# Optimization experiments

Measured on AMD Instinct MI355X. Metric: run time of the kernel, lower is better.

## Reference

```python
import jax, jax.numpy as jnp
import numpy as np

T, B, S = 8, 4, 2048
LAT, SYM, NC = 1024, 256, 512


def setup_inputs() -> dict:
    key = jax.random.key(0)
    ks = jax.random.split(key, 16)
    inp = {
        "token_state": jax.random.normal(ks[0], (B, S, LAT), jnp.float32),
        "bus_symbols": jax.random.normal(ks[1], (T, B, S, SYM), jnp.float32),
        "bus_indices": jax.random.randint(ks[2], (T, B, S), 0, NC),
        "bus_outputs": jax.random.normal(ks[3], (T, B, S, LAT), jnp.float32),
        "bus_mask": jnp.zeros((T,), jnp.bool_),
        # parameters (stored as (in, out) matrices)
        "Wq": jax.random.normal(ks[4], (SYM, 1), jnp.float32) / np.sqrt(SYM),
        "bq": jnp.zeros((1,), jnp.float32),
        "Wread": jax.random.normal(ks[5], (2 * LAT, LAT), jnp.float32) / np.sqrt(2 * LAT),
        "bread": jnp.zeros((LAT,), jnp.float32),
        "Wsym": jax.random.normal(ks[6], (LAT, SYM), jnp.float32) / np.sqrt(LAT),
        "bsym": jnp.zeros((SYM,), jnp.float32),
        "Wc1": jax.random.normal(ks[7], (LAT + SYM, LAT), jnp.float32) / np.sqrt(LAT + SYM),
        "bc1": jnp.zeros((LAT,), jnp.float32),
        "Wc2": jax.random.normal(ks[8], (LAT, LAT), jnp.float32) / np.sqrt(LAT),
        "bc2": jnp.zeros((LAT,), jnp.float32),
        "codebook": jax.random.normal(ks[9], (NC, SYM), jnp.float32),
    }
    return inp


def reference(token_state, bus_symbols, bus_indices, bus_outputs, bus_mask,
              Wq, bq, Wread, bread, Wsym, bsym, Wc1, bc1, Wc2, bc2, codebook):
    Tm, Bb, Ss, Dsym = bus_symbols.shape
    N = Bb * Ss
    syms = bus_symbols.reshape(Tm, N, Dsym)          # [T, N, SYM]
    outs = bus_outputs.reshape(Tm, N, -1)            # [T, N, LAT]

    # top-1 bus message routing
    relevance = (syms @ Wq + bq)[..., 0]             # [T, N]
    top_msg_idx = jnp.argmax(relevance, axis=0)      # [N]
    chosen = jnp.take_along_axis(outs, top_msg_idx[None, :, None], axis=0)[0]  # [N, LAT]
    bus_context = chosen.reshape(Bb, Ss, -1)

    z = jnp.concatenate([token_state, bus_context], axis=-1)
    z_read = z @ Wread + bread                       # [B, S, LAT]
    raw_symbol = z_read @ Wsym + bsym                # [B, S, SYM]

    # VQ: cdist argmin (squared distance has same argmin)
    flat = raw_symbol.reshape(-1, Dsym)              # [N, SYM]
    d2 = (jnp.sum(flat * flat, axis=1, keepdims=True)
          - 2.0 * flat @ codebook.T
          + jnp.sum(codebook * codebook, axis=1)[None, :])  # [N, NC]
    indices = jnp.argmin(d2, axis=-1)                # [N]
    quantized = codebook[indices].reshape(Bb, Ss, Dsym)

    h = jax.nn.relu(jnp.concatenate([z_read, quantized], axis=-1) @ Wc1 + bc1)
    node_output = h @ Wc2 + bc2 + token_state

    used_counts = jnp.zeros((Tm,), jnp.int32).at[top_msg_idx].add(1)
    keep_mask = used_counts == 0
    return node_output, quantized, indices.reshape(Bb, Ss), keep_mask
```

## Files before the change

kernel.cpp:

```cpp
#include <hip/hip_runtime.h>
#include <hip/hip_bf16.h>

#define DEVI __device__ __forceinline__

namespace {

constexpr int T_   = 8;
constexpr int NTOK = 8192;
constexpr int LAT  = 1024;
constexpr int SYM  = 256;
constexpr int NC   = 512;
constexpr float TAU = 0.6f;

typedef short short8 __attribute__((ext_vector_type(8)));
typedef float floatx4 __attribute__((ext_vector_type(4)));

DEVI unsigned short f2bf(float f){
  union { float f; unsigned u; } v; v.f = f;
  return (unsigned short)((v.u + 0x7fffu + ((v.u >> 16) & 1u)) >> 16);
}

DEVI void gload_lds16(const void* g, void* l){
  __builtin_amdgcn_global_load_lds((const __attribute__((address_space(1))) void*)g,
                                   (__attribute__((address_space(3))) void*)l, 16, 0, 0);
}

__global__ void route_k(const float* __restrict__ syms, const float* __restrict__ Wq,
                        int* __restrict__ top, int* __restrict__ counts){
  int gt = blockIdx.x * blockDim.x + threadIdx.x;
  int wid = gt >> 6, lane = gt & 63;
  if (wid >= NTOK) return;
  float4 wq = *(const float4*)(Wq + lane * 4);
  float best = -INFINITY; int bt = 0;
  for (int t = 0; t < T_; ++t){
    float4 s = *(const float4*)(syms + ((size_t)t * NTOK + wid) * SYM + lane * 4);
    float p = s.x*wq.x + s.y*wq.y + s.z*wq.z + s.w*wq.w;
    #pragma unroll
    for (int off = 32; off; off >>= 1) p += __shfl_down(p, off, 64);
    p = __shfl(p, 0, 64);
    if (p > best){ best = p; bt = t; }
  }
  if (lane == 0){ top[wid] = bt; atomicAdd(&counts[bt], 1); }
}

__global__ void mask_k(const int* __restrict__ counts, float* __restrict__ out_mask){
  int t = threadIdx.x;
  if (t < T_) out_mask[t] = (counts[t] == 0) ? 1.0f : 0.0f;
}

__global__ void cbt_k(const float* __restrict__ cb, float* __restrict__ cbT){
  int i = blockIdx.x * blockDim.x + threadIdx.x;
  if (i < NC * SYM){ int c = i / SYM, k = i % SYM; cbT[k * NC + c] = cb[i]; }
}

__global__ void cnorm_k(const float* __restrict__ cb, const float* __restrict__ bsym,
                        float* __restrict__ cnorm, float* __restrict__ svec){
  int gt = blockIdx.x * blockDim.x + threadIdx.x;
  int wid = gt >> 6, lane = gt & 63;
  if (wid >= NC) return;
  float4 v = *(const float4*)(cb + (size_t)wid * SYM + lane * 4);
  float4 b = *(const float4*)(bsym + lane * 4);
  float p = v.x*v.x + v.y*v.y + v.z*v.z + v.w*v.w;
  float q = v.x*(v.x-2.f*b.x) + v.y*(v.y-2.f*b.y) + v.z*(v.z-2.f*b.z) + v.w*(v.w-2.f*b.w);
  #pragma unroll
  for (int off = 32; off; off >>= 1){ p += __shfl_down(p, off, 64); q += __shfl_down(q, off, 64); }
  if (lane == 0){ cnorm[wid] = p; svec[wid] = q; }
}

__global__ void rbias_k(const float* __restrict__ bread, const float* __restrict__ Wsym,
                        const float* __restrict__ bsym, float* __restrict__ rb){
  int t = threadIdx.x;
  float acc = bsym[t];
  for (int k = 0; k < LAT; ++k) acc += bread[k] * Wsym[(size_t)k * SYM + t];
  rb[t] = acc;
}

__global__ void t32_k(const float* __restrict__ in, unsigned short* __restrict__ out,
                      int R, int C){
  __shared__ float tile[32][33];
  int tid = threadIdx.x;
  int tx = tid & 31, ty = tid >> 5;
  int r0 = blockIdx.y * 32, c0 = blockIdx.x * 32;
  #pragma unroll
  for (int j = 0; j < 4; ++j)
    tile[ty + j*8][tx] = in[(size_t)(r0 + ty + j*8) * C + c0 + tx];
  __syncthreads();
  #pragma unroll
  for (int j = 0; j < 4; ++j)
    out[(size_t)(c0 + ty + j*8) * R + r0 + tx] = f2bf(tile[tx][ty + j*8]);
}

__global__ void pack_az(const float* __restrict__ ts, const float* __restrict__ bus,
                        const int* __restrict__ top, unsigned short* __restrict__ Az){
  int id = blockIdx.x * blockDim.x + threadIdx.x;
  int m = id >> 9, c = (id & 511) * 4;
  const float* src = (c < LAT) ? (ts + (size_t)m * LAT + c)
                               : (bus + ((size_t)top[m] * NTOK + m) * LAT + (c - LAT));
  float4 v = *(const float4*)src;
  ushort4 o; o.x = f2bf(v.x); o.y = f2bf(v.y); o.z = f2bf(v.z); o.w = f2bf(v.w);
  *(ushort4*)(Az + (size_t)m * (2*LAT) + c) = o;
}

template<int BM, int BN, int BK, int TM, int TN>
__global__ __launch_bounds__((BM/TM)*(BN/TN))
void gemm_f32(const float* __restrict__ A, const float* __restrict__ Bm,
              float* __restrict__ Cf, int M, int N, int K)
{
  constexpr int NT  = (BM/TM)*(BN/TN);
  constexpr int BMp = BM + 4, BNp = BN + 4;
  constexpr int KV  = BK / 4;
  constexpr int NLA = BM * KV;
  constexpr int NLB = (BK * BN) / 4;
  __shared__ float As[BK][BMp];
  __shared__ float Bs[BK][BNp];
  const int tid = threadIdx.x;
  const int tx = tid % (BN / TN), ty = tid / (BN / TN);
  const int m0 = blockIdx.x * BM, n0 = blockIdx.y * BN;
  float acc[TM][TN] = {};
  for (int k0 = 0; k0 < K; k0 += BK){
    for (int q = tid; q < NLA; q += NT){
      int m = q / KV, kq = (q % KV) * 4;
      float4 v = *(const float4*)(A + (size_t)(m0+m) * K + k0 + kq);
      As[kq+0][m] = v.x; As[kq+1][m] = v.y; As[kq+2][m] = v.z; As[kq+3][m] = v.w;
    }
    for (int q = tid; q < NLB; q += NT){
      int k = q / (BN/4), n4 = (q % (BN/4)) * 4;
      *(float4*)&Bs[k][n4] = *(const float4*)(Bm + (size_t)(k0+k) * N + n0 + n4);
    }
    __syncthreads();
    #pragma unroll
    for (int k = 0; k < BK; ++k){
      float a[TM], b[TN];
      #pragma unroll
      for (int i = 0; i < TM; ++i) a[i] = As[k][ty*TM + i];
      #pragma unroll
      for (int j = 0; j < TN; ++j) b[j] = Bs[k][tx*TN + j];
      #pragma unroll
      for (int i = 0; i < TM; ++i)
        #pragma unroll
        for (int j = 0; j < TN; ++j) acc[i][j] += a[i] * b[j];
    }
    __syncthreads();
  }
  #pragma unroll
  for (int i = 0; i < TM; ++i)
    #pragma unroll
    for (int j = 0; j < TN; ++j)
      Cf[(size_t)(m0 + ty*TM + i) * N + n0 + tx*TN + j] = acc[i][j];
}

constexpr int A_PLAIN = 0, A_CAT = 1;
constexpr int EP_ZH = 0, EP_VQ = 1, EP_RELU = 2, EP_OUT = 3;

template<int ASRC, int EPI>
__global__ __launch_bounds__(256)
void mgemm(const unsigned short* __restrict__ A, const unsigned short* __restrict__ A2,
           const unsigned short* __restrict__ BT, const float* __restrict__ bias,
           const float* __restrict__ resid,
           unsigned short* __restrict__ Cb, float* __restrict__ Cf,
           int N, int K, int asplit)
{
  __shared__ unsigned short As[128*32];
  __shared__ unsigned short Bs[128*32];
  const int tid  = threadIdx.x;
  const int wave = tid >> 6, lane = tid & 63;
  const int wy = wave >> 1, wx = wave & 1;
  const int lq = lane >> 4, lr = lane & 15;
  const int m0 = blockIdx.y * 128, n0 = blockIdx.x * 128;

  floatx4 acc[4][4] = {};

  for (int k0 = 0; k0 < K; k0 += 32){
    #pragma unroll
    for (int c = 0; c < 2; ++c){
      int chunk = tid + c*256;
      int mrel = chunk >> 2, kc = (chunk & 3) * 8;
      int gk = k0 + kc;
      const unsigned short* srcA;
      if constexpr (ASRC == A_CAT){
        if (gk < asplit) srcA = A  + (size_t)(m0+mrel) * asplit + gk;
        else             srcA = A2 + (size_t)(m0+mrel) * (K-asplit) + (gk-asplit);
      } else {
        srcA = A + (size_t)(m0+mrel) * K + gk;
      }
      unsigned short* dstA = &As[(c*256 + wave*64) * 8];
      unsigned short* dstB = &Bs[(c*256 + wave*64) * 8];
      gload_lds16(srcA, dstA);
      gload_lds16(BT + (size_t)(n0+mrel) * K + gk, dstB);
    }
    __syncthreads();
    short8 af[4], bf[4];
    #pragma unroll
    for (int i = 0; i < 4; ++i){
      af[i] = *(const short8*)&As[(wy*64 + i*16 + lr)*32 + lq*8];
      bf[i] = *(const short8*)&Bs[(wx*64 + i*16 + lr)*32 + lq*8];
    }
    #pragma unroll
    for (int i = 0; i < 4; ++i)
      #pragma unroll
      for (int j = 0; j < 4; ++j)
        acc[i][j] = __builtin_amdgcn_mfma_f32_16x16x32_bf16(af[i], bf[j], acc[i][j], 0, 0, 0);
    __syncthreads();
  }

  #pragma unroll
  for (int i = 0; i < 4; ++i){
    #pragma unroll
    for (int j = 0; j < 4; ++j){
      int gn = n0 + wx*64 + j*16 + lr;
      #pragma unroll
      for (int r = 0; r < 4; ++r){
        int gm = m0 + wy*64 + i*16 + lq*4 + r;
        float v = acc[i][j][r];
        if constexpr (EPI == EP_ZH){
          Cb[(size_t)gm * N + gn] = f2bf(v + bias[gn]);
        } else if constexpr (EPI == EP_VQ){
          Cf[(size_t)gm * N + gn] = bias[gn] - 2.f * v;
        } else if constexpr (EPI == EP_RELU){
          float u = v + bias[gn];
          Cb[(size_t)gm * N + gn] = f2bf(u > 0.f ? u : 0.f);
        } else {
          Cf[(size_t)gm * N + gn] = v + bias[gn] + resid[(size_t)gm * N + gn];
        }
      }
    }
  }
}

__global__ void vq_k(const float* __restrict__ scores, const float* __restrict__ cb,
                     float* __restrict__ out_q, float* __restrict__ out_idx,
                     unsigned short* __restrict__ q_h,
                     int* __restrict__ rcount, int* __restrict__ rlist){
  int gt = blockIdx.x * blockDim.x + threadIdx.x;
  int wid = gt >> 6, lane = gt & 63;
  if (wid >= NTOK) return;
  const float* row = scores + (size_t)wid * NC;
  float v1 = INFINITY, v2 = INFINITY; int i1 = 0x7fffffff;
  #pragma unroll
  for (int i = 0; i < NC/64; ++i){
    int c = i*64 + lane;
    float v = row[c];
    if (v < v1){ v2 = v1; v1 = v; i1 = c; } else v2 = fminf(v2, v);
  }
  #pragma unroll
  for (int off = 32; off; off >>= 1){
    float ov1 = __shfl_down(v1, off, 64);
    int   oi1 = __shfl_down(i1, off, 64);
    float ov2 = __shfl_down(v2, off, 64);
    float rest;
    if (ov1 < v1 || (ov1 == v1 && oi1 < i1)){ rest = v1; v1 = ov1; i1 = oi1; }
    else rest = ov1;
    v2 = fminf(fminf(v2, ov2), rest);
  }
  i1 = __shfl(i1, 0, 64);
  if (lane == 0){
    out_idx[wid] = (float)i1;
    if (__shfl(v2, 0, 64) - __shfl(v1, 0, 64) < TAU){
      int p = atomicAdd(rcount, 1); rlist[p] = wid;
    }
  }
  float4 cv = *(const float4*)(cb + (size_t)i1 * SYM + lane * 4);
  *(float4*)(out_q + (size_t)wid * SYM + lane * 4) = cv;
  ushort4 qh; qh.x = f2bf(cv.x); qh.y = f2bf(cv.y); qh.z = f2bf(cv.z); qh.w = f2bf(cv.w);
  *(ushort4*)(q_h + (size_t)wid * SYM + lane * 4) = qh;
}

constexpr int RT = 4;

__global__ __launch_bounds__(256)
void repair_k(const int* __restrict__ rcount, const int* __restrict__ rlist,
              const int* __restrict__ top,
              const float* __restrict__ ts, const float* __restrict__ bus,
              const float* __restrict__ Wcomb, const float* __restrict__ rb,
              const float* __restrict__ cb, const float* __restrict__ cnorm,
              float* __restrict__ out_q, float* __restrict__ out_idx,
              unsigned short* __restrict__ q_h){
  __shared__ float a[RT][2*LAT];
  __shared__ float raw[RT][SYM];
  __shared__ float pv[RT][4];
  __shared__ int   pi[RT][4];
  __shared__ int   fidx[RT];
  int tid = threadIdx.x;
  int lane = tid & 63, wave = tid >> 6;
  int cnt = *rcount;
  int nchunk = (cnt + RT - 1) / RT;
  for (int ch = blockIdx.x; ch < nchunk; ch += gridDim.x){
    int base = ch * RT;
    int nt = min(RT, cnt - base);
    for (int q = tid; q < nt * 512; q += 256){
      int t = q >> 9, c = (q & 511) * 4;
      int m = rlist[base + t];
      int tp = top[m];
      float4 v = (c < LAT) ? *(const float4*)(ts + (size_t)m * LAT + c)
                           : *(const float4*)(bus + ((size_t)tp * NTOK + m) * LAT + (c - LAT));
      *(float4*)&a[t][c] = v;
    }
    __syncthreads();
    float acc0[RT], acc1[RT], acc2[RT], acc3[RT];
    #pragma unroll
    for (int t = 0; t < RT; ++t){ acc0[t]=0.f; acc1[t]=0.f; acc2[t]=0.f; acc3[t]=0.f; }
    for (int k = 0; k < 2*LAT; k += 4){
      float w0 = Wcomb[(size_t)(k+0) * SYM + tid];
      float w1 = Wcomb[(size_t)(k+1) * SYM + tid];
      float w2 = Wcomb[(size_t)(k+2) * SYM + tid];
      float w3 = Wcomb[(size_t)(k+3) * SYM + tid];
      #pragma unroll
      for (int t = 0; t < RT; ++t){
        float4 av = *(const float4*)&a[t][k];
        acc0[t] += av.x * w0; acc1[t] += av.y * w1;
        acc2[t] += av.z * w2; acc3[t] += av.w * w3;
      }
    }
    #pragma unroll
    for (int t = 0; t < RT; ++t)
      raw[t][tid] = rb[tid] + ((acc0[t] + acc1[t]) + (acc2[t] + acc3[t]));
    __syncthreads();
    float bv[RT]; int bi[RT];
    #pragma unroll
    for (int t = 0; t < RT; ++t){ bv[t] = INFINITY; bi[t] = 0x7fffffff; }
    #pragma unroll
    for (int cc = 0; cc < 2; ++cc){
      int c = tid + cc * 256;
      const float* cr = cb + (size_t)c * SYM;
      float d[RT] = {};
      for (int j = 0; j < SYM; j += 4){
        float4 cv = *(const float4*)(cr + j);
        #pragma unroll
        for (int t = 0; t < RT; ++t){
          float4 rv4 = *(const float4*)&raw[t][j];
          d[t] += rv4.x*cv.x + rv4.y*cv.y + rv4.z*cv.z + rv4.w*cv.w;
        }
      }
      #pragma unroll
      for (int t = 0; t < RT; ++t){
        float s = cnorm[c] - 2.f * d[t];
        if (s < bv[t] || (s == bv[t] && c < bi[t])){ bv[t] = s; bi[t] = c; }
      }
    }
    #pragma unroll
    for (int t = 0; t < RT; ++t){
      float v = bv[t]; int i = bi[t];
      #pragma unroll
      for (int off = 32; off; off >>= 1){
        float ov = __shfl_down(v, off, 64);
        int   oi = __shfl_down(i, off, 64);
        if (ov < v || (ov == v && oi < i)){ v = ov; i = oi; }
      }
      if (lane == 0){ pv[t][wave] = v; pi[t][wave] = i; }
    }
    __syncthreads();
    if (tid < nt){
      float v = pv[tid][0]; int i = pi[tid][0];
      #pragma unroll
      for (int w = 1; w < 4; ++w){
        if (pv[tid][w] < v || (pv[tid][w] == v && pi[tid][w] < i)){ v = pv[tid][w]; i = pi[tid][w]; }
      }
      fidx[tid] = i;
      out_idx[rlist[base + tid]] = (float)i;
    }
    __syncthreads();
    for (int t = 0; t < nt; ++t){
      int m = rlist[base + t];
      int idx = fidx[t];
      float cvv = cb[(size_t)idx * SYM + tid];
      out_q[(size_t)m * SYM + tid] = cvv;
      q_h[(size_t)m * SYM + tid] = f2bf(cvv);
    }
    __syncthreads();
  }
}

}

extern "C" void kernel_launch(void* const* d_in, const int* in_sizes, int n_in,
                              void* d_out, int out_size, void* d_ws, size_t ws_size,
                              hipStream_t stream){
  const float* token_state = (const float*)d_in[0];
  const float* bus_symbols = (const float*)d_in[1];
  const float* bus_outputs = (const float*)d_in[3];
  const float* Wq    = (const float*)d_in[5];
  const float* Wread = (const float*)d_in[7];
  const float* bread = (const float*)d_in[8];
  const float* Wsym  = (const float*)d_in[9];
  const float* bsym  = (const float*)d_in[10];
  const float* Wc1   = (const float*)d_in[11];
  const float* bc1   = (const float*)d_in[12];
  const float* Wc2   = (const float*)d_in[13];
  const float* bc2   = (const float*)d_in[14];
  const float* codebook = (const float*)d_in[15];

  float* out_node = (float*)d_out;
  float* out_quant= out_node + (size_t)NTOK * LAT;
  float* out_idx  = out_quant + (size_t)NTOK * SYM;
  float* out_mask = out_idx + NTOK;

  char* W = (char*)d_ws; size_t off = 0;
  auto alloc = [&](size_t bytes)->char*{ char* p = W + off; off = (off + bytes + 255) & ~(size_t)255; return p; };
  int*   top     = (int*)alloc(NTOK*4);
  int*   counts  = (int*)alloc(64);
  int*   rcount  = (int*)alloc(64);
  int*   rlist   = (int*)alloc(NTOK*4);
  float* cbT     = (float*)alloc((size_t)SYM*NC*4);
  float* cnorm   = (float*)alloc(NC*4);
  float* svec    = (float*)alloc(NC*4);
  float* rb      = (float*)alloc(SYM*4);
  float* Wfuse   = (float*)alloc((size_t)LAT*NC*4);
  float* Wcomb   = (float*)alloc((size_t)2*LAT*SYM*4);
  unsigned short* WreadT = (unsigned short*)alloc((size_t)LAT*2*LAT*2);
  unsigned short* Wc1T   = (unsigned short*)alloc((size_t)LAT*(LAT+SYM)*2);
  unsigned short* Wc2T   = (unsigned short*)alloc((size_t)LAT*LAT*2);
  unsigned short* WfuseT = (unsigned short*)alloc((size_t)NC*LAT*2);
  unsigned short* z_h    = (unsigned short*)alloc((size_t)NTOK*LAT*2);
  unsigned short* q_h    = (unsigned short*)alloc((size_t)NTOK*SYM*2);
  unsigned short* h_h    = (unsigned short*)alloc((size_t)NTOK*LAT*2);
  char* az_region        = alloc((size_t)NTOK*2*LAT*2);
  unsigned short* A_z    = (unsigned short*)az_region;
  float* scores          = (float*)az_region;

  hipMemsetAsync(counts, 0, T_*sizeof(int), stream);
  hipMemsetAsync(rcount, 0, sizeof(int), stream);

  route_k<<<NTOK/4, 256, 0, stream>>>(bus_symbols, Wq, top, counts);
  mask_k<<<1, 64, 0, stream>>>(counts, out_mask);
  cbt_k<<<(NC*SYM)/256, 256, 0, stream>>>(codebook, cbT);
  cnorm_k<<<NC/4, 256, 0, stream>>>(codebook, bsym, cnorm, svec);
  rbias_k<<<1, SYM, 0, stream>>>(bread, Wsym, bsym, rb);

  gemm_f32<64,64,8,4,4><<<dim3(LAT/64, NC/64), 256, 0, stream>>>(Wsym, cbT, Wfuse, LAT, NC, SYM);
  t32_k<<<dim3(NC/32, LAT/32), 256, 0, stream>>>(Wfuse, WfuseT, LAT, NC);
  gemm_f32<32,64,8,2,4><<<dim3(2*LAT/32, SYM/64), 256, 0, stream>>>(Wread, Wsym, Wcomb, 2*LAT, SYM, LAT);
  t32_k<<<dim3(LAT/32, 2*LAT/32), 256, 0, stream>>>(Wread, WreadT, 2*LAT, LAT);
  t32_k<<<dim3(LAT/32, (LAT+SYM)/32), 256, 0, stream>>>(Wc1, Wc1T, LAT+SYM, LAT);
  t32_k<<<dim3(LAT/32, LAT/32), 256, 0, stream>>>(Wc2, Wc2T, LAT, LAT);

  pack_az<<<(NTOK*512)/256, 256, 0, stream>>>(token_state, bus_outputs, top, A_z);

  mgemm<A_PLAIN, EP_ZH><<<dim3(LAT/128, NTOK/128), 256, 0, stream>>>(
      A_z, nullptr, WreadT, bread, nullptr, z_h, nullptr, LAT, 2*LAT, 0);
  mgemm<A_PLAIN, EP_VQ><<<dim3(NC/128, NTOK/128), 256, 0, stream>>>(
      z_h, nullptr, WfuseT, svec, nullptr, nullptr, scores, NC, LAT, 0);

  vq_k<<<NTOK/4, 256, 0, stream>>>(scores, codebook, out_quant, out_idx, q_h, rcount, rlist);
  repair_k<<<512, 256, 0, stream>>>(rcount, rlist, top, token_state, bus_outputs,
                                    Wcomb, rb, codebook, cnorm, out_quant, out_idx, q_h);

  mgemm<A_CAT, EP_RELU><<<dim3(LAT/128, NTOK/128), 256, 0, stream>>>(
      z_h, q_h, Wc1T, bc1, nullptr, h_h, nullptr, LAT, LAT+SYM, LAT);
  mgemm<A_PLAIN, EP_OUT><<<dim3(LAT/128, NTOK/128), 256, 0, stream>>>(
      h_h, nullptr, Wc2T, bc2, token_state, nullptr, out_node, LAT, LAT, 0);
}
```

Before: 925.3 us.

## Fuse A-packing into first GEMM and merge small setup kernels

Removes the pack_az pass by having the first MFMA GEMM load fp32 token_state and gathered bus_outputs directly, convert them to bf16 in registers and store them to LDS. Small kernels are merged into fewer launches: mask into cbt, rbias into cnorm, and the three transposes into one. The fused-weight GEMM now writes a transposed bf16 result directly. The memsets are combined into one. This cuts launch overhead and a full round-trip of the packed activation, but the first GEMM's A load is no longer asynchronous global-to-LDS and reads twice the bytes in fp32.

Result: slower. 966.5 us (+4.4%).

```diff
diff --git a/kernel.cpp b/kernel.cpp
--- a/kernel.cpp
+++ b/kernel.cpp
@@ -43,18 +43,30 @@
   if (lane == 0){ top[wid] = bt; atomicAdd(&counts[bt], 1); }
 }
 
-__global__ void mask_k(const int* __restrict__ counts, float* __restrict__ out_mask){
-  int t = threadIdx.x;
-  if (t < T_) out_mask[t] = (counts[t] == 0) ? 1.0f : 0.0f;
-}
-
-__global__ void cbt_k(const float* __restrict__ cb, float* __restrict__ cbT){
+__global__ void cbt_k(const float* __restrict__ cb, float* __restrict__ cbT,
+                      const int* __restrict__ counts, float* __restrict__ out_mask){
   int i = blockIdx.x * blockDim.x + threadIdx.x;
   if (i < NC * SYM){ int c = i / SYM, k = i % SYM; cbT[k * NC + c] = cb[i]; }
+  if (blockIdx.x == 0 && threadIdx.x < T_)
+    out_mask[threadIdx.x] = (counts[threadIdx.x] == 0) ? 1.0f : 0.0f;
 }
 
 __global__ void cnorm_k(const float* __restrict__ cb, const float* __restrict__ bsym,
-                        float* __restrict__ cnorm, float* __restrict__ svec){
+                        float* __restrict__ cnorm, float* __restrict__ svec,
+                        const float* __restrict__ bread, const float* __restrict__ Wsym,
+                        float* __restrict__ rb){
+  if (blockIdx.x == NC/4){
+    int t = threadIdx.x;
+    float a0=0.f,a1=0.f,a2=0.f,a3=0.f;
+    for (int k = 0; k < LAT; k += 4){
+      a0 += bread[k+0] * Wsym[(size_t)(k+0) * SYM + t];
+      a1 += bread[k+1] * Wsym[(size_t)(k+1) * SYM + t];
+      a2 += bread[k+2] * Wsym[(size_t)(k+2) * SYM + t];
+      a3 += bread[k+3] * Wsym[(size_t)(k+3) * SYM + t];
+    }
+    rb[t] = bsym[t] + ((a0+a1)+(a2+a3));
+    return;
+  }
   int gt = blockIdx.x * blockDim.x + threadIdx.x;
   int wid = gt >> 6, lane = gt & 63;
   if (wid >= NC) return;
@@ -67,20 +79,19 @@
   if (lane == 0){ cnorm[wid] = p; svec[wid] = q; }
 }
 
-__global__ void rbias_k(const float* __restrict__ bread, const float* __restrict__ Wsym,
-                        const float* __restrict__ bsym, float* __restrict__ rb){
-  int t = threadIdx.x;
-  float acc = bsym[t];
-  for (int k = 0; k < LAT; ++k) acc += bread[k] * Wsym[(size_t)k * SYM + t];
-  rb[t] = acc;
-}
-
-__global__ void t32_k(const float* __restrict__ in, unsigned short* __restrict__ out,
-                      int R, int C){
+__global__ void t32multi_k(const float* __restrict__ Wread, unsigned short* __restrict__ WreadT,
+                           const float* __restrict__ Wc1,   unsigned short* __restrict__ Wc1T,
+                           const float* __restrict__ Wc2,   unsigned short* __restrict__ Wc2T){
   __shared__ float tile[32][33];
+  int b = blockIdx.x;
+  const float* in; unsigned short* out; int R, C, t;
+  if (b < 2048){ in = Wread; out = WreadT; R = 2*LAT; C = LAT; t = b; }
+  else if (b < 2048+1280){ in = Wc1; out = Wc1T; R = LAT+SYM; C = LAT; t = b - 2048; }
+  else { in = Wc2; out = Wc2T; R = LAT; C = LAT; t = b - 3328; }
+  int bx = t % 32, by = t / 32;
+  int r0 = by * 32, c0 = bx * 32;
   int tid = threadIdx.x;
   int tx = tid & 31, ty = tid >> 5;
-  int r0 = blockIdx.y * 32, c0 = blockIdx.x * 32;
   #pragma unroll
   for (int j = 0; j < 4; ++j)
     tile[ty + j*8][tx] = in[(size_t)(r0 + ty + j*8) * C + c0 + tx];
@@ -90,21 +101,11 @@
     out[(size_t)(c0 + ty + j*8) * R + r0 + tx] = f2bf(tile[tx][ty + j*8]);
 }
 
-__global__ void pack_az(const float* __restrict__ ts, const float* __restrict__ bus,
-                        const int* __restrict__ top, unsigned short* __restrict__ Az){
-  int id = blockIdx.x * blockDim.x + threadIdx.x;
-  int m = id >> 9, c = (id & 511) * 4;
-  const float* src = (c < LAT) ? (ts + (size_t)m * LAT + c)
-                               : (bus + ((size_t)top[m] * NTOK + m) * LAT + (c - LAT));
-  float4 v = *(const float4*)src;
-  ushort4 o; o.x = f2bf(v.x); o.y = f2bf(v.y); o.z = f2bf(v.z); o.w = f2bf(v.w);
-  *(ushort4*)(Az + (size_t)m * (2*LAT) + c) = o;
-}
-
-template<int BM, int BN, int BK, int TM, int TN>
+template<int BM, int BN, int BK, int TM, int TN, int TB>
 __global__ __launch_bounds__((BM/TM)*(BN/TN))
 void gemm_f32(const float* __restrict__ A, const float* __restrict__ Bm,
-              float* __restrict__ Cf, int M, int N, int K)
+              float* __restrict__ Cf, unsigned short* __restrict__ Ct,
+              int M, int N, int K)
 {
   constexpr int NT  = (BM/TM)*(BN/TN);
   constexpr int BMp = BM + 4, BNp = BN + 4;
@@ -145,11 +146,16 @@
   #pragma unroll
   for (int i = 0; i < TM; ++i)
     #pragma unroll
-    for (int j = 0; j < TN; ++j)
-      Cf[(size_t)(m0 + ty*TM + i) * N + n0 + tx*TN + j] = acc[i][j];
-}
-
-constexpr int A_PLAIN = 0, A_CAT = 1;
+    for (int j = 0; j < TN; ++j){
+      if constexpr (TB){
+        Ct[(size_t)(n0 + tx*TN + j) * M + m0 + ty*TM + i] = f2bf(acc[i][j]);
+      } else {
+        Cf[(size_t)(m0 + ty*TM + i) * N + n0 + tx*TN + j] = acc[i][j];
+      }
+    }
+}
+
+constexpr int A_PLAIN = 0, A_CAT = 1, A_F32CAT = 2;
 constexpr int EP_ZH = 0, EP_VQ = 1, EP_RELU = 2, EP_OUT = 3;
 
 template<int ASRC, int EPI>
@@ -158,16 +164,24 @@
            const unsigned short* __restrict__ BT, const float* __restrict__ bias,
            const float* __restrict__ resid,
            unsigned short* __restrict__ Cb, float* __restrict__ Cf,
-           int N, int K, int asplit)
+           int N, int K, int asplit,
+           const float* __restrict__ Af, const float* __restrict__ A2f,
+           const int* __restrict__ topp)
 {
   __shared__ unsigned short As[128*32];
   __shared__ unsigned short Bs[128*32];
+  __shared__ int topl[128];
   const int tid  = threadIdx.x;
   const int wave = tid >> 6, lane = tid & 63;
   const int wy = wave >> 1, wx = wave & 1;
   const int lq = lane >> 4, lr = lane & 15;
   const int m0 = blockIdx.y * 128, n0 = blockIdx.x * 128;
 
+  if constexpr (ASRC == A_F32CAT){
+    if (tid < 128) topl[tid] = topp[m0 + tid];
+    __syncthreads();
+  }
+
   floatx4 acc[4][4] = {};
 
   for (int k0 = 0; k0 < K; k0 += 32){
@@ -176,17 +190,27 @@
       int chunk = tid + c*256;
       int mrel = chunk >> 2, kc = (chunk & 3) * 8;
       int gk = k0 + kc;
-      const unsigned short* srcA;
-      if constexpr (ASRC == A_CAT){
-        if (gk < asplit) srcA = A  + (size_t)(m0+mrel) * asplit + gk;
-        else             srcA = A2 + (size_t)(m0+mrel) * (K-asplit) + (gk-asplit);
+      if constexpr (ASRC == A_F32CAT){
+        const float* sf;
+        if (gk < asplit) sf = Af + (size_t)(m0+mrel) * asplit + gk;
+        else sf = A2f + ((size_t)topl[mrel] * NTOK + (m0+mrel)) * (size_t)(K-asplit) + (gk-asplit);
+        float4 v0 = *(const float4*)sf;
+        float4 v1 = *(const float4*)(sf + 4);
+        short8 o;
+        o[0]=(short)f2bf(v0.x); o[1]=(short)f2bf(v0.y); o[2]=(short)f2bf(v0.z); o[3]=(short)f2bf(v0.w);
+        o[4]=(short)f2bf(v1.x); o[5]=(short)f2bf(v1.y); o[6]=(short)f2bf(v1.z); o[7]=(short)f2bf(v1.w);
+        *(short8*)&As[chunk*8] = o;
       } else {
-        srcA = A + (size_t)(m0+mrel) * K + gk;
-      }
-      unsigned short* dstA = &As[(c*256 + wave*64) * 8];
-      unsigned short* dstB = &Bs[(c*256 + wave*64) * 8];
-      gload_lds16(srcA, dstA);
-      gload_lds16(BT + (size_t)(n0+mrel) * K + gk, dstB);
+        const unsigned short* srcA;
+        if constexpr (ASRC == A_CAT){
+          if (gk < asplit) srcA = A  + (size_t)(m0+mrel) * asplit + gk;
+          else             srcA = A2 + (size_t)(m0+mrel) * (K-asplit) + (gk-asplit);
+        } else {
+          srcA = A + (size_t)(m0+mrel) * K + gk;
+        }
+        gload_lds16(srcA, &As[(c*256 + wave*64) * 8]);
+      }
+      gload_lds16(BT + (size_t)(n0+mrel) * K + gk, &Bs[(c*256 + wave*64) * 8]);
     }
     __syncthreads();
     short8 af[4], bf[4];
@@ -397,14 +421,14 @@
   char* W = (char*)d_ws; size_t off = 0;
   auto alloc = [&](size_t bytes)->char*{ char* p = W + off; off = (off + bytes + 255) & ~(size_t)255; return p; };
   int*   top     = (int*)alloc(NTOK*4);
-  int*   counts  = (int*)alloc(64);
-  int*   rcount  = (int*)alloc(64);
+  char*  zeroed  = alloc(256);
+  int*   counts  = (int*)zeroed;
+  int*   rcount  = (int*)(zeroed + 128);
   int*   rlist   = (int*)alloc(NTOK*4);
   float* cbT     = (float*)alloc((size_t)SYM*NC*4);
   float* cnorm   = (float*)alloc(NC*4);
   float* svec    = (float*)alloc(NC*4);
   float* rb      = (float*)alloc(SYM*4);
-  float* Wfuse   = (float*)alloc((size_t)LAT*NC*4);
   float* Wcomb   = (float*)alloc((size_t)2*LAT*SYM*4);
   unsigned short* WreadT = (unsigned short*)alloc((size_t)LAT*2*LAT*2);
   unsigned short* Wc1T   = (unsigned short*)alloc((size_t)LAT*(LAT+SYM)*2);
@@ -413,39 +437,35 @@
   unsigned short* z_h    = (unsigned short*)alloc((size_t)NTOK*LAT*2);
   unsigned short* q_h    = (unsigned short*)alloc((size_t)NTOK*SYM*2);
   unsigned short* h_h    = (unsigned short*)alloc((size_t)NTOK*LAT*2);
-  char* az_region        = alloc((size_t)NTOK*2*LAT*2);
-  unsigned short* A_z    = (unsigned short*)az_region;
-  float* scores          = (float*)az_region;
-
-  hipMemsetAsync(counts, 0, T_*sizeof(int), stream);
-  hipMemsetAsync(rcount, 0, sizeof(int), stream);
+  float* scores          = (float*)alloc((size_t)NTOK*NC*4);
+
+  hipMemsetAsync(zeroed, 0, 256, stream);
 
   route_k<<<NTOK/4, 256, 0, stream>>>(bus_symbols, Wq, top, counts);
-  mask_k<<<1, 64, 0, stream>>>(counts, out_mask);
-  cbt_k<<<(NC*SYM)/256, 256, 0, stream>>>(codebook, cbT);
-  cnorm_k<<<NC/4, 256, 0, stream>>>(codebook, bsym, cnorm, svec);
-  rbias_k<<<1, SYM, 0, stream>>>(bread, Wsym, bsym, rb);
-
-  gemm_f32<64,64,8,4,4><<<dim3(LAT/64, NC/64), 256, 0, stream>>>(Wsym, cbT, Wfuse, LAT, NC, SYM);
-  t32_k<<<dim3(NC/32, LAT/32), 256, 0, stream>>>(Wfuse, WfuseT, LAT, NC);
-  gemm_f32<32,64,8,2,4><<<dim3(2*LAT/32, SYM/64), 256, 0, stream>>>(Wread, Wsym, Wcomb, 2*LAT, SYM, LAT);
-  t32_k<<<dim3(LAT/32, 2*LAT/32), 256, 0, stream>>>(Wread, WreadT, 2*LAT, LAT);
-  t32_k<<<dim3(LAT/32, (LAT+SYM)/32), 256, 0, stream>>>(Wc1, Wc1T, LAT+SYM, LAT);
-  t32_k<<<dim3(LAT/32, LAT/32), 256, 0, stream>>>(Wc2, Wc2T, LAT, LAT);
-
-  pack_az<<<(NTOK*512)/256, 256, 0, stream>>>(token_state, bus_outputs, top, A_z);
-
-  mgemm<A_PLAIN, EP_ZH><<<dim3(LAT/128, NTOK/128), 256, 0, stream>>>(
-      A_z, nullptr, WreadT, bread, nullptr, z_h, nullptr, LAT, 2*LAT, 0);
+  cbt_k<<<(NC*SYM)/256, 256, 0, stream>>>(codebook, cbT, counts, out_mask);
+  cnorm_k<<<NC/4 + 1, 256, 0, stream>>>(codebook, bsym, cnorm, svec, bread, Wsym, rb);
+
+  gemm_f32<64,64,8,4,4,1><<<dim3(LAT/64, NC/64), 256, 0, stream>>>(
+      Wsym, cbT, nullptr, WfuseT, LAT, NC, SYM);
+  gemm_f32<32,64,8,2,4,0><<<dim3(2*LAT/32, SYM/64), 256, 0, stream>>>(
+      Wread, Wsym, Wcomb, nullptr, 2*LAT, SYM, LAT);
+  t32multi_k<<<2048+1280+1024, 256, 0, stream>>>(Wread, WreadT, Wc1, Wc1T, Wc2, Wc2T);
+
+  mgemm<A_F32CAT, EP_ZH><<<dim3(LAT/128, NTOK/128), 256, 0, stream>>>(
+      nullptr, nullptr, WreadT, bread, nullptr, z_h, nullptr, LAT, 2*LAT, LAT,
+      token_state, bus_outputs, top);
   mgemm<A_PLAIN, EP_VQ><<<dim3(NC/128, NTOK/128), 256, 0, stream>>>(
-      z_h, nullptr, WfuseT, svec, nullptr, nullptr, scores, NC, LAT, 0);
+      z_h, nullptr, WfuseT, svec, nullptr, nullptr, scores, NC, LAT, 0,
+      nullptr, nullptr, nullptr);
 
   vq_k<<<NTOK/4, 256, 0, stream>>>(scores, codebook, out_quant, out_idx, q_h, rcount, rlist);
   repair_k<<<512, 256, 0, stream>>>(rcount, rlist, top, token_state, bus_outputs,
                                     Wcomb, rb, codebook, cnorm, out_quant, out_idx, q_h);
 
   mgemm<A_CAT, EP_RELU><<<dim3(LAT/128, NTOK/128), 256, 0, stream>>>(
-      z_h, q_h, Wc1T, bc1, nullptr, h_h, nullptr, LAT, LAT+SYM, LAT);
+      z_h, q_h, Wc1T, bc1, nullptr, h_h, nullptr, LAT, LAT+SYM, LAT,
+      nullptr, nullptr, nullptr);
   mgemm<A_PLAIN, EP_OUT><<<dim3(LAT/128, NTOK/128), 256, 0, stream>>>(
-      h_h, nullptr, Wc2T, bc2, token_state, nullptr, out_node, LAT, LAT, 0);
-}
+      h_h, nullptr, Wc2T, bc2, token_state, nullptr, out_node, LAT, LAT, 0,
+      nullptr, nullptr, nullptr);
+}
```
